# Kernel optimization log

Hardware: AMD Instinct MI355X
Metric: run time of the kernel (lower is better)

The kernel has to match this reference:

```python
import jax, jax.numpy as jnp
import numpy as np

D_MODEL = 1024
NUM_HEADS = 16
HEAD_DIM = D_MODEL // NUM_HEADS


def setup_inputs() -> dict:
    key = jax.random.key(0)
    ks = jax.random.split(key, 12)
    B, S = 4, 2048
    inp = {
        "query": jax.random.normal(ks[0], (B, S, D_MODEL), jnp.float32),
        "key": jax.random.normal(ks[1], (B, S, D_MODEL), jnp.float32),
        "value": jax.random.normal(ks[2], (B, S, D_MODEL), jnp.float32),
        "mask": jnp.ones((B, 1, S, S), dtype=bool),
    }
    sc = 1.0 / np.sqrt(D_MODEL)
    inp["Wq"] = jax.random.normal(ks[3], (D_MODEL, D_MODEL), jnp.float32) * sc
    inp["bq"] = jnp.zeros((D_MODEL,), jnp.float32)
    inp["Wk"] = jax.random.normal(ks[4], (D_MODEL, D_MODEL), jnp.float32) * sc
    inp["bk"] = jnp.zeros((D_MODEL,), jnp.float32)
    inp["Wv"] = jax.random.normal(ks[5], (D_MODEL, D_MODEL), jnp.float32) * sc
    inp["bv"] = jnp.zeros((D_MODEL,), jnp.float32)
    inp["Wo"] = jax.random.normal(ks[6], (D_MODEL, D_MODEL), jnp.float32) * sc
    inp["bo"] = jnp.zeros((D_MODEL,), jnp.float32)
    return inp


def reference(query, key, value, mask, Wq, bq, Wk, bk, Wv, bv, Wo, bo):
    B, S, _ = query.shape
    H, hd = NUM_HEADS, HEAD_DIM

    def proj(x, W, b):
        # [B,S,D] @ [D,D] -> [B,S,H,hd] -> [B,H,S,hd]
        return (x @ W + b).reshape(B, S, H, hd).transpose(0, 2, 1, 3)

    q = proj(query, Wq, bq)
    k = proj(key, Wk, bk)
    v = proj(value, Wv, bv)

    scores = jnp.einsum("bhqd,bhkd->bhqk", q, k) / jnp.sqrt(jnp.float32(hd))
    scores = jnp.where(mask, scores, jnp.float32(-jnp.inf))
    attn = jax.nn.softmax(scores, axis=-1)  # dropout p=0 (eval) -> identity
    ctx = jnp.einsum("bhqk,bhkd->bhqd", attn, v)
    ctx = ctx.transpose(0, 2, 1, 3).reshape(B, S, H * hd)
    return ctx @ Wo + bo
```

## Files before the change

### kernel.cpp

```cpp
#include <hip/hip_runtime.h>
#include <stdint.h>
#include <math.h>

#define DMODEL 1024
#define NHEADS 16
#define HDIM   64
#define BATCH  4
#define SEQ    2048
#define MROWS  (BATCH*SEQ)

typedef float  f32x4  __attribute__((ext_vector_type(4)));
typedef short  short8 __attribute__((ext_vector_type(8)));

static __device__ __forceinline__ unsigned short f2bf(float f) {
  unsigned int u = __builtin_bit_cast(unsigned int, f);
  u = u + 0x7FFFu + ((u >> 16) & 1u);
  return (unsigned short)(u >> 16);
}

#define GLOAD16(gp, lp)                                                        \
  __builtin_amdgcn_global_load_lds(                                            \
      (const __attribute__((address_space(1))) void*)(gp),                     \
      (__attribute__((address_space(3))) void*)(lp), 16, 0, 0)

__global__ __launch_bounds__(256) void cvt_x_kernel(const float* __restrict__ in,
                                                    unsigned short* __restrict__ out) {
  size_t i = ((size_t)blockIdx.x * 256 + threadIdx.x) * 8;
  float4 a = *(const float4*)(in + i);
  float4 b = *(const float4*)(in + i + 4);
  short8 o;
  o[0] = (short)f2bf(a.x); o[1] = (short)f2bf(a.y);
  o[2] = (short)f2bf(a.z); o[3] = (short)f2bf(a.w);
  o[4] = (short)f2bf(b.x); o[5] = (short)f2bf(b.y);
  o[6] = (short)f2bf(b.z); o[7] = (short)f2bf(b.w);
  *(short8*)(out + i) = o;
}

__global__ __launch_bounds__(256) void cvt_w_kernel(const float* __restrict__ Wq,
                                                    const float* __restrict__ Wk,
                                                    const float* __restrict__ Wv,
                                                    const float* __restrict__ Wo,
                                                    unsigned short* __restrict__ wt) {
  __shared__ float tile[32][33];
  const float* W = (blockIdx.z == 0) ? Wq : (blockIdx.z == 1) ? Wk
                 : (blockIdx.z == 2) ? Wv : Wo;
  unsigned short* out = wt + (size_t)blockIdx.z * DMODEL * DMODEL;
  int tx = threadIdx.x & 31, ty = threadIdx.x >> 5;
  int r0 = blockIdx.y * 32, c0 = blockIdx.x * 32;
#pragma unroll
  for (int j = 0; j < 4; j++)
    tile[ty + j * 8][tx] = W[(size_t)(r0 + ty + j * 8) * DMODEL + c0 + tx];
  __syncthreads();
#pragma unroll
  for (int j = 0; j < 4; j++)
    out[(size_t)(c0 + ty + j * 8) * DMODEL + r0 + tx] = f2bf(tile[tx][ty + j * 8]);
}

__global__ __launch_bounds__(256, 2) void gemm_bf16_kernel(
    const unsigned short* __restrict__ A, const unsigned short* __restrict__ Bt,
    const float* __restrict__ bias, void* __restrict__ dst, int mode, float scale) {
  __shared__ unsigned short As[128 * 32];
  __shared__ unsigned short Bs[128 * 32];
  const int tid  = threadIdx.x;
  const int lane = tid & 63, wid = tid >> 6;
  const int row0 = blockIdx.x * 128, col0 = blockIdx.y * 128;
  const int wm = (wid >> 1) * 64, wn = (wid & 1) * 64;
  const int fr = lane & 15, fk8 = (lane >> 4) * 8;

  f32x4 acc[4][4] = {};

  for (int kt = 0; kt < DMODEL / 32; ++kt) {
    __syncthreads();
    const int k0 = kt * 32;
#pragma unroll
    for (int i = 0; i < 2; ++i) {
      int t = i * 256 + tid;
      int r = t >> 2, c = (t & 3) * 8;
      GLOAD16(A  + (size_t)(row0 + r) * DMODEL + k0 + c, &As[t * 8]);
      GLOAD16(Bt + (size_t)(col0 + r) * DMODEL + k0 + c, &Bs[t * 8]);
    }
    __syncthreads();
    short8 fa[4], fb[4];
#pragma unroll
    for (int mi = 0; mi < 4; mi++)
      fa[mi] = *(const short8*)&As[(wm + mi * 16 + fr) * 32 + fk8];
#pragma unroll
    for (int ni = 0; ni < 4; ni++)
      fb[ni] = *(const short8*)&Bs[(wn + ni * 16 + fr) * 32 + fk8];
#pragma unroll
    for (int mi = 0; mi < 4; mi++)
#pragma unroll
      for (int ni = 0; ni < 4; ni++)
        acc[mi][ni] = __builtin_amdgcn_mfma_f32_16x16x32_bf16(fa[mi], fb[ni],
                                                              acc[mi][ni], 0, 0, 0);
  }

#pragma unroll
  for (int ni = 0; ni < 4; ni++) {
    int gn = col0 + wn + ni * 16 + fr;
    float bv = bias[gn];
#pragma unroll
    for (int mi = 0; mi < 4; mi++) {
#pragma unroll
      for (int r = 0; r < 4; r++) {
        int gm = row0 + wm + mi * 16 + (lane >> 4) * 4 + r;
        float c = (acc[mi][ni][r] + bv) * scale;
        if (mode == 2) {
          ((float*)dst)[(size_t)gm * DMODEL + gn] = c;
        } else {
          int b = gm >> 11, s = gm & 2047, h = gn >> 6, d = gn & 63;
          size_t off = (mode == 0)
                           ? ((size_t)((b * NHEADS + h) * SEQ + s) * HDIM + d)
                           : ((size_t)((b * NHEADS + h) * HDIM + d) * SEQ + s);
          ((unsigned short*)dst)[off] = f2bf(c);
        }
      }
    }
  }
}

__global__ __launch_bounds__(256, 2) void flash_attn_kernel(
    const unsigned short* __restrict__ Qb,
    const unsigned short* __restrict__ Kb,
    const unsigned short* __restrict__ Vtb,
    unsigned short* __restrict__ ctx) {
  __shared__ unsigned short Ks[2][64 * 64];
  __shared__ unsigned short Vs[2][64 * 64];
  __shared__ unsigned short Ps[4][16 * 64];

  const int tid = threadIdx.x, lane = tid & 63, wid = tid >> 6;
  const int bh = blockIdx.y;
  const int q0 = blockIdx.x * 64 + wid * 16;
  const unsigned short* Qh = Qb  + (size_t)bh * SEQ * HDIM;
  const unsigned short* Kh = Kb  + (size_t)bh * SEQ * HDIM;
  const unsigned short* Vh = Vtb + (size_t)bh * HDIM * SEQ;
  const int fr = lane & 15, fk8 = (lane >> 4) * 8;

  short8 qf[2];
  qf[0] = *(const short8*)&Qh[(size_t)(q0 + fr) * HDIM + fk8];
  qf[1] = *(const short8*)&Qh[(size_t)(q0 + fr) * HDIM + 32 + fk8];

  f32x4 oacc[4] = {};
  float mrun[4], lsum[4];
#pragma unroll
  for (int r = 0; r < 4; r++) { mrun[r] = -INFINITY; lsum[r] = 0.f; }

  auto stage = [&](int buf, int t) {
    const int kv0 = t * 64;
#pragma unroll
    for (int i = 0; i < 2; ++i) {
      int tt = i * 256 + tid;
      int r = tt >> 3;
      int cs = ((tt & 7) ^ (r & 7)) * 8;
      GLOAD16(Kh + (size_t)(kv0 + r) * HDIM + cs, &Ks[buf][tt * 8]);
      GLOAD16(Vh + (size_t)r * SEQ + kv0 + cs,    &Vs[buf][tt * 8]);
    }
  };

  stage(0, 0);
  const int NT = SEQ / 64;
  for (int t = 0; t < NT; ++t) {
    const int buf = t & 1;
    __syncthreads();
    if (t + 1 < NT) stage(buf ^ 1, t + 1);

    f32x4 sf[4];
#pragma unroll
    for (int ni = 0; ni < 4; ni++) {
      int row = ni * 16 + fr;
      int sw = (row & 7) << 4;
      const char* kbase = (const char*)&Ks[buf][0] + row * 128;
      short8 b0 = *(const short8*)(kbase + ((fk8 * 2) ^ sw));
      short8 b1 = *(const short8*)(kbase + ((64 + fk8 * 2) ^ sw));
      f32x4 z = {};
      z = __builtin_amdgcn_mfma_f32_16x16x32_bf16(qf[0], b0, z, 0, 0, 0);
      z = __builtin_amdgcn_mfma_f32_16x16x32_bf16(qf[1], b1, z, 0, 0, 0);
      sf[ni] = z;
    }

    float pv[4][4];
#pragma unroll
    for (int r = 0; r < 4; r++) {
      float tm = fmaxf(fmaxf(sf[0][r], sf[1][r]), fmaxf(sf[2][r], sf[3][r]));
#pragma unroll
      for (int off = 8; off >= 1; off >>= 1)
        tm = fmaxf(tm, __shfl_xor(tm, off, 16));
      float mn = fmaxf(mrun[r], tm);
      float al = __expf(mrun[r] - mn);
      float rs = 0.f;
#pragma unroll
      for (int ni = 0; ni < 4; ni++) {
        float p = __expf(sf[ni][r] - mn);
        pv[r][ni] = p; rs += p;
      }
#pragma unroll
      for (int off = 8; off >= 1; off >>= 1)
        rs += __shfl_xor(rs, off, 16);
      lsum[r] = lsum[r] * al + rs;
      mrun[r] = mn;
#pragma unroll
      for (int ni = 0; ni < 4; ni++) oacc[ni][r] *= al;
    }

    char* pbase = (char*)&Ps[wid][0];
#pragma unroll
    for (int ni = 0; ni < 4; ni++) {
#pragma unroll
      for (int r = 0; r < 4; r++) {
        int prow = (lane >> 4) * 4 + r;
        int pcolb = (ni * 16 + fr) * 2;
        *(unsigned short*)(pbase + prow * 128 + (pcolb ^ ((prow & 7) << 4))) =
            f2bf(pv[r][ni]);
      }
    }
    __syncthreads();

#pragma unroll
    for (int ks = 0; ks < 2; ks++) {
      int inb = (ks * 64 + fk8 * 2) ^ ((fr & 7) << 4);
      short8 pa = *(const short8*)((const char*)&Ps[wid][0] + fr * 128 + inb);
#pragma unroll
      for (int ni = 0; ni < 4; ni++) {
        int vrow = ni * 16 + fr;
        int vin = (ks * 64 + fk8 * 2) ^ ((vrow & 7) << 4);
        short8 vb = *(const short8*)((const char*)&Vs[buf][0] + vrow * 128 + vin);
        oacc[ni] = __builtin_amdgcn_mfma_f32_16x16x32_bf16(pa, vb, oacc[ni], 0, 0, 0);
      }
    }
  }

  const int b = bh >> 4, h = bh & 15;
#pragma unroll
  for (int r = 0; r < 4; r++) {
    float inv = 1.0f / lsum[r];
    int q = q0 + (lane >> 4) * 4 + r;
#pragma unroll
    for (int ni = 0; ni < 4; ni++) {
      int d = ni * 16 + fr;
      ctx[((size_t)(b * SEQ + q)) * DMODEL + h * HDIM + d] = f2bf(oacc[ni][r] * inv);
    }
  }
}

extern "C" void kernel_launch(void* const* d_in, const int* in_sizes, int n_in,
                              void* d_out, int out_size, void* d_ws, size_t ws_size,
                              hipStream_t stream) {
  (void)in_sizes; (void)n_in; (void)out_size; (void)ws_size;
  const float* query = (const float*)d_in[0];
  const float* key   = (const float*)d_in[1];
  const float* value = (const float*)d_in[2];
  const float* Wq = (const float*)d_in[4];  const float* bq = (const float*)d_in[5];
  const float* Wk = (const float*)d_in[6];  const float* bk = (const float*)d_in[7];
  const float* Wv = (const float*)d_in[8];  const float* bv = (const float*)d_in[9];
  const float* Wo = (const float*)d_in[10]; const float* bo = (const float*)d_in[11];
  float* out = (float*)d_out;

  char* ws = (char*)d_ws;
  unsigned short* Xbf = (unsigned short*)(ws);
  unsigned short* WT  = (unsigned short*)(ws + (16u << 20));
  unsigned short* Qb  = (unsigned short*)(ws + (24u << 20));
  unsigned short* Kb  = (unsigned short*)(ws + (40u << 20));
  unsigned short* Vb  = (unsigned short*)(ws + (56u << 20));

  unsigned short* WTq = WT;
  unsigned short* WTk = WT + (size_t)DMODEL * DMODEL;
  unsigned short* WTv = WT + 2 * (size_t)DMODEL * DMODEL;
  unsigned short* WTo = WT + 3 * (size_t)DMODEL * DMODEL;

  const dim3 gemm_grid(MROWS / 128, DMODEL / 128);
  const int cvt_blocks = (MROWS * DMODEL) / (256 * 8);

  cvt_w_kernel<<<dim3(32, 32, 4), 256, 0, stream>>>(Wq, Wk, Wv, Wo, WT);

  cvt_x_kernel<<<cvt_blocks, 256, 0, stream>>>(query, Xbf);
  gemm_bf16_kernel<<<gemm_grid, 256, 0, stream>>>(Xbf, WTq, bq, Qb, 0, 0.125f);
  cvt_x_kernel<<<cvt_blocks, 256, 0, stream>>>(key, Xbf);
  gemm_bf16_kernel<<<gemm_grid, 256, 0, stream>>>(Xbf, WTk, bk, Kb, 0, 1.0f);
  cvt_x_kernel<<<cvt_blocks, 256, 0, stream>>>(value, Xbf);
  gemm_bf16_kernel<<<gemm_grid, 256, 0, stream>>>(Xbf, WTv, bv, Vb, 1, 1.0f);

  flash_attn_kernel<<<dim3(SEQ / 64, BATCH * NHEADS), 256, 0, stream>>>(Qb, Kb, Vb, Xbf);

  gemm_bf16_kernel<<<gemm_grid, 256, 0, stream>>>(Xbf, WTo, bo, out, 2, 1.0f);
}
```

Baseline: 517.7 us.

## Rewrite flash attention with 32x32 MFMA, register P, lazy rescale; double-buffer GEMM

```diff
diff --git a/kernel.cpp b/kernel.cpp
--- a/kernel.cpp
+++ b/kernel.cpp
@@ -9,14 +9,22 @@
 #define SEQ    2048
 #define MROWS  (BATCH*SEQ)
 
-typedef float  f32x4  __attribute__((ext_vector_type(4)));
-typedef short  short8 __attribute__((ext_vector_type(8)));
+typedef float  f32x4   __attribute__((ext_vector_type(4)));
+typedef float  f32x16  __attribute__((ext_vector_type(16)));
+typedef short  short8  __attribute__((ext_vector_type(8)));
 
 static __device__ __forceinline__ unsigned short f2bf(float f) {
   unsigned int u = __builtin_bit_cast(unsigned int, f);
   u = u + 0x7FFFu + ((u >> 16) & 1u);
   return (unsigned short)(u >> 16);
 }
+
+static __device__ __forceinline__ int cvtpk_bf16(float lo, float hi) {
+  int d;
+  asm("v_cvt_pk_bf16_f32 %0, %1, %2" : "=v"(d) : "v"(lo), "v"(hi));
+  return d;
+}
+#define PLSWAP(a, b) asm("v_permlane32_swap_b32 %0, %1" : "+v"(a), "+v"(b))
 
 #define GLOAD16(gp, lp)                                                        \
   __builtin_amdgcn_global_load_lds(                                            \
@@ -59,8 +67,8 @@
 __global__ __launch_bounds__(256, 2) void gemm_bf16_kernel(
     const unsigned short* __restrict__ A, const unsigned short* __restrict__ Bt,
     const float* __restrict__ bias, void* __restrict__ dst, int mode, float scale) {
-  __shared__ unsigned short As[128 * 32];
-  __shared__ unsigned short Bs[128 * 32];
+  __shared__ unsigned short As[2][128 * 32];
+  __shared__ unsigned short Bs[2][128 * 32];
   const int tid  = threadIdx.x;
   const int lane = tid & 63, wid = tid >> 6;
   const int row0 = blockIdx.x * 128, col0 = blockIdx.y * 128;
@@ -69,24 +77,29 @@
 
   f32x4 acc[4][4] = {};
 
-  for (int kt = 0; kt < DMODEL / 32; ++kt) {
-    __syncthreads();
+  auto stage = [&](int buf, int kt) {
     const int k0 = kt * 32;
 #pragma unroll
     for (int i = 0; i < 2; ++i) {
       int t = i * 256 + tid;
       int r = t >> 2, c = (t & 3) * 8;
-      GLOAD16(A  + (size_t)(row0 + r) * DMODEL + k0 + c, &As[t * 8]);
-      GLOAD16(Bt + (size_t)(col0 + r) * DMODEL + k0 + c, &Bs[t * 8]);
-    }
+      GLOAD16(A  + (size_t)(row0 + r) * DMODEL + k0 + c, &As[buf][t * 8]);
+      GLOAD16(Bt + (size_t)(col0 + r) * DMODEL + k0 + c, &Bs[buf][t * 8]);
+    }
+  };
+  stage(0, 0);
+
+  for (int kt = 0; kt < DMODEL / 32; ++kt) {
+    const int buf = kt & 1;
     __syncthreads();
+    if (kt + 1 < DMODEL / 32) stage(buf ^ 1, kt + 1);
     short8 fa[4], fb[4];
 #pragma unroll
     for (int mi = 0; mi < 4; mi++)
-      fa[mi] = *(const short8*)&As[(wm + mi * 16 + fr) * 32 + fk8];
+      fa[mi] = *(const short8*)&As[buf][(wm + mi * 16 + fr) * 32 + fk8];
 #pragma unroll
     for (int ni = 0; ni < 4; ni++)
-      fb[ni] = *(const short8*)&Bs[(wn + ni * 16 + fr) * 32 + fk8];
+      fb[ni] = *(const short8*)&Bs[buf][(wn + ni * 16 + fr) * 32 + fk8];
 #pragma unroll
     for (int mi = 0; mi < 4; mi++)
 #pragma unroll
@@ -98,147 +111,147 @@
 #pragma unroll
   for (int ni = 0; ni < 4; ni++) {
     int gn = col0 + wn + ni * 16 + fr;
-    float bv = bias[gn];
 #pragma unroll
     for (int mi = 0; mi < 4; mi++) {
 #pragma unroll
       for (int r = 0; r < 4; r++) {
         int gm = row0 + wm + mi * 16 + (lane >> 4) * 4 + r;
-        float c = (acc[mi][ni][r] + bv) * scale;
         if (mode == 2) {
-          ((float*)dst)[(size_t)gm * DMODEL + gn] = c;
+          ((float*)dst)[(size_t)gm * DMODEL + gn] = acc[mi][ni][r] + bias[gn];
+        } else if (mode == 0) {
+          float c = (acc[mi][ni][r] + bias[gn]) * scale;
+          int b = gm >> 11, s = gm & 2047, h = gn >> 6, d = gn & 63;
+          ((unsigned short*)dst)[(size_t)((b * NHEADS + h) * SEQ + s) * HDIM + d] =
+              f2bf(c);
         } else {
-          int b = gm >> 11, s = gm & 2047, h = gn >> 6, d = gn & 63;
-          size_t off = (mode == 0)
-                           ? ((size_t)((b * NHEADS + h) * SEQ + s) * HDIM + d)
-                           : ((size_t)((b * NHEADS + h) * HDIM + d) * SEQ + s);
-          ((unsigned short*)dst)[off] = f2bf(c);
+          float c = acc[mi][ni][r] + bias[gm];
+          int h = gm >> 6, d = gm & 63, b = gn >> 11, s = gn & 2047;
+          ((unsigned short*)dst)[(size_t)((b * NHEADS + h) * HDIM + d) * SEQ + s] =
+              f2bf(c);
         }
       }
     }
   }
 }
 
-__global__ __launch_bounds__(256, 2) void flash_attn_kernel(
+__global__ __launch_bounds__(512, 2) void flash_attn_kernel(
     const unsigned short* __restrict__ Qb,
     const unsigned short* __restrict__ Kb,
     const unsigned short* __restrict__ Vtb,
     unsigned short* __restrict__ ctx) {
   __shared__ unsigned short Ks[2][64 * 64];
   __shared__ unsigned short Vs[2][64 * 64];
-  __shared__ unsigned short Ps[4][16 * 64];
 
   const int tid = threadIdx.x, lane = tid & 63, wid = tid >> 6;
+  const int cl = lane & 31, hi = lane >> 5;
   const int bh = blockIdx.y;
-  const int q0 = blockIdx.x * 64 + wid * 16;
+  const int qwb = blockIdx.x * 256 + wid * 32;
   const unsigned short* Qh = Qb  + (size_t)bh * SEQ * HDIM;
   const unsigned short* Kh = Kb  + (size_t)bh * SEQ * HDIM;
   const unsigned short* Vh = Vtb + (size_t)bh * HDIM * SEQ;
-  const int fr = lane & 15, fk8 = (lane >> 4) * 8;
-
-  short8 qf[2];
-  qf[0] = *(const short8*)&Qh[(size_t)(q0 + fr) * HDIM + fk8];
-  qf[1] = *(const short8*)&Qh[(size_t)(q0 + fr) * HDIM + 32 + fk8];
-
-  f32x4 oacc[4] = {};
-  float mrun[4], lsum[4];
-#pragma unroll
-  for (int r = 0; r < 4; r++) { mrun[r] = -INFINITY; lsum[r] = 0.f; }
-
+
+  short8 qf[4];
+#pragma unroll
+  for (int ks = 0; ks < 4; ks++)
+    qf[ks] = *(const short8*)&Qh[(size_t)(qwb + cl) * HDIM + ks * 16 + hi * 8];
+
+  f32x16 oa0 = {}, oa1 = {};
+  float m = -INFINITY, l = 0.f;
+
+  const int r_st = tid >> 3;
+  const int c_st = (tid & 7) ^ (r_st & 7);
   auto stage = [&](int buf, int t) {
     const int kv0 = t * 64;
-#pragma unroll
-    for (int i = 0; i < 2; ++i) {
-      int tt = i * 256 + tid;
-      int r = tt >> 3;
-      int cs = ((tt & 7) ^ (r & 7)) * 8;
-      GLOAD16(Kh + (size_t)(kv0 + r) * HDIM + cs, &Ks[buf][tt * 8]);
-      GLOAD16(Vh + (size_t)r * SEQ + kv0 + cs,    &Vs[buf][tt * 8]);
-    }
+    GLOAD16(Kh + (size_t)(kv0 + r_st) * HDIM + c_st * 8, &Ks[buf][tid * 8]);
+    GLOAD16(Vh + (size_t)r_st * SEQ + kv0 + c_st * 8,    &Vs[buf][tid * 8]);
   };
-
   stage(0, 0);
+
+  const int sw = (cl & 7) << 4;
   const int NT = SEQ / 64;
   for (int t = 0; t < NT; ++t) {
     const int buf = t & 1;
     __syncthreads();
     if (t + 1 < NT) stage(buf ^ 1, t + 1);
 
-    f32x4 sf[4];
-#pragma unroll
-    for (int ni = 0; ni < 4; ni++) {
-      int row = ni * 16 + fr;
-      int sw = (row & 7) << 4;
-      const char* kbase = (const char*)&Ks[buf][0] + row * 128;
-      short8 b0 = *(const short8*)(kbase + ((fk8 * 2) ^ sw));
-      short8 b1 = *(const short8*)(kbase + ((64 + fk8 * 2) ^ sw));
-      f32x4 z = {};
-      z = __builtin_amdgcn_mfma_f32_16x16x32_bf16(qf[0], b0, z, 0, 0, 0);
-      z = __builtin_amdgcn_mfma_f32_16x16x32_bf16(qf[1], b1, z, 0, 0, 0);
-      sf[ni] = z;
-    }
-
-    float pv[4][4];
-#pragma unroll
-    for (int r = 0; r < 4; r++) {
-      float tm = fmaxf(fmaxf(sf[0][r], sf[1][r]), fmaxf(sf[2][r], sf[3][r]));
-#pragma unroll
-      for (int off = 8; off >= 1; off >>= 1)
-        tm = fmaxf(tm, __shfl_xor(tm, off, 16));
-      float mn = fmaxf(mrun[r], tm);
-      float al = __expf(mrun[r] - mn);
-      float rs = 0.f;
-#pragma unroll
-      for (int ni = 0; ni < 4; ni++) {
-        float p = __expf(sf[ni][r] - mn);
-        pv[r][ni] = p; rs += p;
+    const char* kb = (const char*)&Ks[buf][0];
+    const char* vbp = (const char*)&Vs[buf][0];
+
+    f32x16 sa0 = {}, sa1 = {};
+#pragma unroll
+    for (int ks = 0; ks < 4; ks++) {
+      int boff = (ks * 32 + hi * 16) ^ sw;
+      short8 ka0 = *(const short8*)(kb + cl * 128 + boff);
+      short8 ka1 = *(const short8*)(kb + (32 + cl) * 128 + boff);
+      sa0 = __builtin_amdgcn_mfma_f32_32x32x16_bf16(ka0, qf[ks], sa0, 0, 0, 0);
+      sa1 = __builtin_amdgcn_mfma_f32_32x32x16_bf16(ka1, qf[ks], sa1, 0, 0, 0);
+    }
+
+    float pmax = sa0[0];
+#pragma unroll
+    for (int i = 1; i < 16; i++) pmax = fmaxf(pmax, sa0[i]);
+#pragma unroll
+    for (int i = 0; i < 16; i++) pmax = fmaxf(pmax, sa1[i]);
+    pmax = fmaxf(pmax, __shfl_xor(pmax, 32));
+    if (__any(pmax > m + 3.f)) {
+      float mn = fmaxf(m, pmax);
+      float al = exp2f(m - mn);
+      l *= al;
+#pragma unroll
+      for (int reg = 0; reg < 16; reg++) {
+        float ar = __shfl(al, (reg & 3) + 8 * (reg >> 2) + 4 * hi);
+        oa0[reg] *= ar; oa1[reg] *= ar;
       }
-#pragma unroll
-      for (int off = 8; off >= 1; off >>= 1)
-        rs += __shfl_xor(rs, off, 16);
-      lsum[r] = lsum[r] * al + rs;
-      mrun[r] = mn;
-#pragma unroll
-      for (int ni = 0; ni < 4; ni++) oacc[ni][r] *= al;
-    }
-
-    char* pbase = (char*)&Ps[wid][0];
-#pragma unroll
-    for (int ni = 0; ni < 4; ni++) {
-#pragma unroll
-      for (int r = 0; r < 4; r++) {
-        int prow = (lane >> 4) * 4 + r;
-        int pcolb = (ni * 16 + fr) * 2;
-        *(unsigned short*)(pbase + prow * 128 + (pcolb ^ ((prow & 7) << 4))) =
-            f2bf(pv[r][ni]);
-      }
-    }
-    __syncthreads();
-
-#pragma unroll
-    for (int ks = 0; ks < 2; ks++) {
-      int inb = (ks * 64 + fk8 * 2) ^ ((fr & 7) << 4);
-      short8 pa = *(const short8*)((const char*)&Ps[wid][0] + fr * 128 + inb);
-#pragma unroll
-      for (int ni = 0; ni < 4; ni++) {
-        int vrow = ni * 16 + fr;
-        int vin = (ks * 64 + fk8 * 2) ^ ((vrow & 7) << 4);
-        short8 vb = *(const short8*)((const char*)&Vs[buf][0] + vrow * 128 + vin);
-        oacc[ni] = __builtin_amdgcn_mfma_f32_16x16x32_bf16(pa, vb, oacc[ni], 0, 0, 0);
-      }
+      m = mn;
+    }
+    float p0[16], p1[16], ps = 0.f;
+#pragma unroll
+    for (int i = 0; i < 16; i++) { p0[i] = exp2f(sa0[i] - m); ps += p0[i]; }
+#pragma unroll
+    for (int i = 0; i < 16; i++) { p1[i] = exp2f(sa1[i] - m); ps += p1[i]; }
+    ps += __shfl_xor(ps, 32);
+    l += ps;
+
+    int w[16];
+#pragma unroll
+    for (int i = 0; i < 8; i++) w[i]     = cvtpk_bf16(p0[2 * i], p0[2 * i + 1]);
+#pragma unroll
+    for (int i = 0; i < 8; i++) w[8 + i] = cvtpk_bf16(p1[2 * i], p1[2 * i + 1]);
+    int afr[4][4];
+#pragma unroll
+    for (int kvt = 0; kvt < 2; kvt++) {
+      int a0 = w[kvt * 8 + 0], a2 = w[kvt * 8 + 2]; PLSWAP(a0, a2);
+      int a1 = w[kvt * 8 + 1], a3 = w[kvt * 8 + 3]; PLSWAP(a1, a3);
+      afr[kvt * 2][0] = a0; afr[kvt * 2][1] = a1;
+      afr[kvt * 2][2] = a2; afr[kvt * 2][3] = a3;
+      int b0 = w[kvt * 8 + 4], b2 = w[kvt * 8 + 6]; PLSWAP(b0, b2);
+      int b1 = w[kvt * 8 + 5], b3 = w[kvt * 8 + 7]; PLSWAP(b1, b3);
+      afr[kvt * 2 + 1][0] = b0; afr[kvt * 2 + 1][1] = b1;
+      afr[kvt * 2 + 1][2] = b2; afr[kvt * 2 + 1][3] = b3;
+    }
+
+#pragma unroll
+    for (int ks = 0; ks < 4; ks++) {
+      union { int i[4]; short8 s; } u;
+      u.i[0] = afr[ks][0]; u.i[1] = afr[ks][1];
+      u.i[2] = afr[ks][2]; u.i[3] = afr[ks][3];
+      int boff = (ks * 32 + hi * 16) ^ sw;
+      short8 vb0 = *(const short8*)(vbp + cl * 128 + boff);
+      short8 vb1 = *(const short8*)(vbp + (32 + cl) * 128 + boff);
+      oa0 = __builtin_amdgcn_mfma_f32_32x32x16_bf16(u.s, vb0, oa0, 0, 0, 0);
+      oa1 = __builtin_amdgcn_mfma_f32_32x32x16_bf16(u.s, vb1, oa1, 0, 0, 0);
     }
   }
 
   const int b = bh >> 4, h = bh & 15;
-#pragma unroll
-  for (int r = 0; r < 4; r++) {
-    float inv = 1.0f / lsum[r];
-    int q = q0 + (lane >> 4) * 4 + r;
-#pragma unroll
-    for (int ni = 0; ni < 4; ni++) {
-      int d = ni * 16 + fr;
-      ctx[((size_t)(b * SEQ + q)) * DMODEL + h * HDIM + d] = f2bf(oacc[ni][r] * inv);
-    }
+  float linv = 1.0f / l;
+#pragma unroll
+  for (int reg = 0; reg < 16; reg++) {
+    int qrow = (reg & 3) + 8 * (reg >> 2) + 4 * hi;
+    float li = __shfl(linv, qrow);
+    size_t base = ((size_t)(b * SEQ + qwb + qrow)) * DMODEL + h * HDIM;
+    ctx[base + cl]      = f2bf(oa0[reg] * li);
+    ctx[base + 32 + cl] = f2bf(oa1[reg] * li);
   }
 }
 
@@ -268,18 +281,20 @@
   unsigned short* WTo = WT + 3 * (size_t)DMODEL * DMODEL;
 
   const dim3 gemm_grid(MROWS / 128, DMODEL / 128);
+  const dim3 gemmT_grid(DMODEL / 128, MROWS / 128);
   const int cvt_blocks = (MROWS * DMODEL) / (256 * 8);
 
   cvt_w_kernel<<<dim3(32, 32, 4), 256, 0, stream>>>(Wq, Wk, Wv, Wo, WT);
 
+  const float qscale = 0.125f * 1.4426950408889634f;
   cvt_x_kernel<<<cvt_blocks, 256, 0, stream>>>(query, Xbf);
-  gemm_bf16_kernel<<<gemm_grid, 256, 0, stream>>>(Xbf, WTq, bq, Qb, 0, 0.125f);
+  gemm_bf16_kernel<<<gemm_grid, 256, 0, stream>>>(Xbf, WTq, bq, Qb, 0, qscale);
   cvt_x_kernel<<<cvt_blocks, 256, 0, stream>>>(key, Xbf);
   gemm_bf16_kernel<<<gemm_grid, 256, 0, stream>>>(Xbf, WTk, bk, Kb, 0, 1.0f);
   cvt_x_kernel<<<cvt_blocks, 256, 0, stream>>>(value, Xbf);
-  gemm_bf16_kernel<<<gemm_grid, 256, 0, stream>>>(Xbf, WTv, bv, Vb, 1, 1.0f);
-
-  flash_attn_kernel<<<dim3(SEQ / 64, BATCH * NHEADS), 256, 0, stream>>>(Qb, Kb, Vb, Xbf);
+  gemm_bf16_kernel<<<gemmT_grid, 256, 0, stream>>>(WTv, Xbf, bv, Vb, 1, 1.0f);
+
+  flash_attn_kernel<<<dim3(SEQ / 256, BATCH * NHEADS), 512, 0, stream>>>(Qb, Kb, Vb, Xbf);
 
   gemm_bf16_kernel<<<gemm_grid, 256, 0, stream>>>(Xbf, WTo, bo, out, 2, 1.0f);
 }
```

Measured after the change: 463.0 us. 1.12x faster.
